# Performance work log

Hardware: AMD Instinct MI355X
Metric: run time of the kernel (lower is better)

## Reference

```python
import jax, jax.numpy as jnp
import numpy as np

B, S, D, DO, L, E = 8, 2048, 256, 256, 8, 32768


def setup_inputs() -> dict:
    key = jax.random.key(0)
    k1, k2, k3, k4, k5, k6 = jax.random.split(key, 6)
    node_repr = jax.random.normal(k1, (B, S, D), dtype=jnp.float32)
    edge_src = jax.random.randint(k2, (B, E), 0, S, dtype=jnp.int32)
    edge_tgt = jax.random.randint(k3, (B, E), 0, S, dtype=jnp.int32)
    edge_label = jax.random.randint(k4, (B, E), 0, L, dtype=jnp.int32)
    # per-label Linear params (torch default: kaiming-ish uniform; values here are random stand-ins)
    bound = 1.0 / np.sqrt(D)
    W = jax.random.uniform(k5, (L, D, DO), dtype=jnp.float32, minval=-bound, maxval=bound)
    b = jax.random.uniform(k6, (L, DO), dtype=jnp.float32, minval=-bound, maxval=bound)
    return {"node_repr": node_repr, "edge_src": edge_src, "edge_tgt": edge_tgt,
            "edge_label": edge_label, "W": W, "b": b}


def reference(node_repr, edge_src, edge_tgt, edge_label, W, b):
    # Transform every node by every label's linear once: y[b,l,s,:] = x[b,s,:] @ W[l] + b[l]
    y = jnp.einsum('bsd,ldo->blso', node_repr, W) + b[None, :, None, :]  # [B,L,S,DO]
    bidx = jnp.arange(node_repr.shape[0])[:, None]                       # [B,1]
    msgs = y[bidx, edge_label, edge_src]                                 # [B,E,DO] gather
    out = jnp.zeros(node_repr.shape[:2] + (W.shape[-1],), dtype=node_repr.dtype)
    out = out.at[bidx, edge_tgt].add(msgs)                               # scatter-add into targets
    return jax.nn.relu(out)
```

## Files before the change

### kernel.cpp

```cpp
#include <hip/hip_runtime.h>
#include <stdint.h>

constexpr int NB = 8;
constexpr int NS = 2048;
constexpr int ND = 256;
constexpr int NDO = 256;
constexpr int NL = 8;
constexpr int NE = 32768;
constexpr int K2 = NL * ND;
constexpr int CAP = 32;

typedef __attribute__((ext_vector_type(8))) short bf16x8;
typedef __attribute__((ext_vector_type(4))) float f32x4;
typedef unsigned int u32;

__device__ __forceinline__ float bf2f(uint32_t u) {
    return __uint_as_float(u << 16);
}
__device__ __forceinline__ uint16_t f2bf(float f) {
    uint32_t x = __float_as_uint(f);
    uint32_t r = (x + 0x7fffu + ((x >> 16) & 1u)) >> 16;
    return (uint16_t)r;
}

__device__ __forceinline__ void gl_lds16(const void* gptr, void* lptr) {
    __builtin_amdgcn_global_load_lds(
        (const __attribute__((address_space(1))) u32*)gptr,
        (__attribute__((address_space(3))) u32*)lptr, 16, 0, 0);
}

__global__ __launch_bounds__(256) void part_kernel(
    const float* __restrict__ W, ushort* __restrict__ wt2,
    const int* __restrict__ esrc, const int* __restrict__ etgt,
    const int* __restrict__ elab,
    int* __restrict__ cursor, ushort* __restrict__ bucket) {
    int bid = blockIdx.x;
    int tid = threadIdx.x;
    if (bid < 1024) {
        int i = bid * 256 + tid;
        int b = i >> 15;
        int c = (b << 14) + etgt[i] * NL + elab[i];
        int p = atomicAdd(&cursor[c], 1);
        if (p < CAP) bucket[(size_t)c * CAP + p] = (ushort)esrc[i];
    } else {
        __shared__ float tile[64][65];
        int tb = bid - 1024;
        int kt = tb & 31, ot = tb >> 5;
        int k0 = kt * 64, o0 = ot * 64;
        int rr = tid >> 6;
        int cc = tid & 63;
        for (int r16 = 0; r16 < 16; r16++) {
            int row = r16 * 4 + rr;
            tile[row][cc] = W[(size_t)(k0 + row) * NDO + o0 + cc];
        }
        __syncthreads();
        for (int r16 = 0; r16 < 16; r16++) {
            int orow = r16 * 4 + rr;
            wt2[(size_t)(o0 + orow) * K2 + k0 + cc] = f2bf(tile[cc][orow]);
        }
    }
}

__global__ __launch_bounds__(256) void agg_kernel(
    const float* __restrict__ x,
    const int* __restrict__ cursor, const ushort* __restrict__ bucket,
    ushort* __restrict__ Z) {
    int bid = blockIdx.x;
    int b = bid & 7;
    int lane = threadIdx.x & 63;
    int t = (bid >> 3) * 4 + (threadIdx.x >> 6);
    int g = b * NS + t;

    int cv = (lane < 8) ? cursor[(g << 3) + lane] : 0;

    const ushort* bp = bucket + (size_t)g * (NL * CAP);
    int my[4];
#pragma unroll
    for (int c = 0; c < 4; c++) my[c] = bp[c * 64 + lane];

    const float4* x4 = (const float4*)x + (size_t)b * NS * 64;
    ushort* zrow = Z + (size_t)g * K2;

#pragma unroll
    for (int l = 0; l < 8; l++) {
        int n = __shfl(cv, l);
        if (n > CAP) n = CAP;
        float4 a; a.x = a.y = a.z = a.w = 0.f;
        for (int q = 0; q < n; q++) {
            int src = __shfl(my[l >> 1], (l & 1) * CAP + q);
            float4 xv = x4[(size_t)src * 64 + lane];
            a.x += xv.x; a.y += xv.y; a.z += xv.z; a.w += xv.w;
        }
        ushort4 ob;
        ob.x = f2bf(a.x); ob.y = f2bf(a.y); ob.z = f2bf(a.z); ob.w = f2bf(a.w);
        ((ushort4*)(zrow + l * ND))[lane] = ob;
    }
}

__global__ __launch_bounds__(256, 4) void gemm2_kernel(
    const ushort* __restrict__ Z, const ushort* __restrict__ wt2,
    const int* __restrict__ cursor, const float* __restrict__ bias,
    float* __restrict__ out) {
    int bid = blockIdx.x;
    int wgid = (bid & 7) * 128 + (bid >> 3);
    int mt = wgid >> 2;
    int n0 = (wgid & 3) * 64;
    int m0 = mt * 64;

    __shared__ ushort As[64 * 64];
    __shared__ ushort Bs[64 * 64];
    __shared__ int cnt_s[64 * 8];
    __shared__ float bias_s[8 * 64];

    int tid = threadIdx.x;
    int lane = tid & 63;
    int wave = __builtin_amdgcn_readfirstlane(tid >> 6);
    int wm = wave & 1, wn = wave >> 1;
    int ln = lane & 15, quad = lane >> 4;

    {
        int e = tid * 2;
        *(int2*)&cnt_s[e] = *(const int2*)&cursor[(size_t)m0 * 8 + e];
        int l = e >> 6, col = e & 63;
        *(float2*)&bias_s[e] = *(const float2*)&bias[l * NDO + n0 + col];
    }

    f32x4 acc[2][2] = {};

    const ushort* Ag = Z + (size_t)m0 * K2;
    const ushort* Bg = wt2 + (size_t)n0 * K2;

    for (int k0 = 0; k0 < K2; k0 += 64) {
#pragma unroll
        for (int p = 0; p < 2; p++) {
            int cid = p * 256 + tid;
            int r = cid >> 3, ch = (cid & 7) ^ (r & 7);
            gl_lds16(Ag + (size_t)r * K2 + k0 + ch * 8, &As[(p * 256 + wave * 64) * 8]);
        }
#pragma unroll
        for (int p = 0; p < 2; p++) {
            int cid = p * 256 + tid;
            int r = cid >> 3, ch = (cid & 7) ^ (r & 7);
            gl_lds16(Bg + (size_t)r * K2 + k0 + ch * 8, &Bs[(p * 256 + wave * 64) * 8]);
        }
        __syncthreads();

#pragma unroll
        for (int ks = 0; ks < 2; ks++) {
            bf16x8 af[2], bfr[2];
#pragma unroll
            for (int i = 0; i < 2; i++) {
                int row = wm * 32 + i * 16 + ln;
                int ci = (ks * 4 + quad) ^ (row & 7);
                af[i] = *(const bf16x8*)&As[row * 64 + ci * 8];
            }
#pragma unroll
            for (int j = 0; j < 2; j++) {
                int row = wn * 32 + j * 16 + ln;
                int ci = (ks * 4 + quad) ^ (row & 7);
                bfr[j] = *(const bf16x8*)&Bs[row * 64 + ci * 8];
            }
#pragma unroll
            for (int i = 0; i < 2; i++)
#pragma unroll
                for (int j = 0; j < 2; j++)
                    acc[i][j] = __builtin_amdgcn_mfma_f32_16x16x32_bf16(
                        af[i], bfr[j], acc[i][j], 0, 0, 0);
        }
        __syncthreads();
    }

#pragma unroll
    for (int i = 0; i < 2; i++) {
#pragma unroll
        for (int r = 0; r < 4; r++) {
            int row_l = wm * 32 + i * 16 + quad * 4 + r;
            float cw[8];
#pragma unroll
            for (int l = 0; l < 8; l++) cw[l] = (float)cnt_s[row_l * 8 + l];
#pragma unroll
            for (int j = 0; j < 2; j++) {
                int col_l = wn * 32 + j * 16 + ln;
                float bs = 0.f;
#pragma unroll
                for (int l = 0; l < 8; l++) bs += cw[l] * bias_s[l * 64 + col_l];
                float v = acc[i][j][r] + bs;
                out[(size_t)(m0 + row_l) * NDO + n0 + col_l] = fmaxf(v, 0.f);
            }
        }
    }
}

extern "C" void kernel_launch(void* const* d_in, const int* in_sizes, int n_in,
                              void* d_out, int out_size, void* d_ws, size_t ws_size,
                              hipStream_t stream) {
    const float* x    = (const float*)d_in[0];
    const int*   esrc = (const int*)d_in[1];
    const int*   etgt = (const int*)d_in[2];
    const int*   elab = (const int*)d_in[3];
    const float* W    = (const float*)d_in[4];
    const float* bias = (const float*)d_in[5];
    float* out = (float*)d_out;

    char* ws = (char*)d_ws;
    ushort* wt2    = (ushort*)(ws);
    int*    cursor = (int*)(ws + 1048576);
    ushort* bucket = (ushort*)(ws + 1572864);
    ushort* Z      = (ushort*)(ws + 10485760);

    hipMemsetAsync(cursor, 0, NB * NS * NL * sizeof(int), stream);
    part_kernel<<<1152, 256, 0, stream>>>(W, wt2, esrc, etgt, elab, cursor, bucket);
    agg_kernel<<<4096, 256, 0, stream>>>(x, cursor, bucket, Z);
    gemm2_kernel<<<1024, 256, 0, stream>>>(Z, wt2, cursor, bias, out);
}
```

Before: 136.5 us.

## Double-buffer GEMM LDS tiles, pair label loops in aggregation, interleave partition batches

The GEMM kernel now double-buffers the A/B LDS tiles, prefetching the next K-tile with global_load_lds while MFMAs run on the current one, so each K step needs one barrier instead of two. The aggregation kernel handles two labels per iteration with independent accumulators, putting more gather loads in flight per wave. The partition kernel maps consecutive blocks to different batches, which spreads atomics across the cursor array. These changes double the GEMM's LDS use, which may cut occupancy. The double-buffering also leans on the single trailing barrier to order the async LDS writes against reads of the other buffer.

```diff
diff --git a/kernel.cpp b/kernel.cpp
--- a/kernel.cpp
+++ b/kernel.cpp
@@ -37,8 +37,8 @@
     int bid = blockIdx.x;
     int tid = threadIdx.x;
     if (bid < 1024) {
-        int i = bid * 256 + tid;
-        int b = i >> 15;
+        int b = bid & 7;
+        int i = b * NE + (bid >> 3) * 256 + tid;
         int c = (b << 14) + etgt[i] * NL + elab[i];
         int p = atomicAdd(&cursor[c], 1);
         if (p < CAP) bucket[(size_t)c * CAP + p] = (ushort)esrc[i];
@@ -82,18 +82,30 @@
     ushort* zrow = Z + (size_t)g * K2;
 
 #pragma unroll
-    for (int l = 0; l < 8; l++) {
-        int n = __shfl(cv, l);
-        if (n > CAP) n = CAP;
-        float4 a; a.x = a.y = a.z = a.w = 0.f;
-        for (int q = 0; q < n; q++) {
-            int src = __shfl(my[l >> 1], (l & 1) * CAP + q);
-            float4 xv = x4[(size_t)src * 64 + lane];
-            a.x += xv.x; a.y += xv.y; a.z += xv.z; a.w += xv.w;
+    for (int lp = 0; lp < 4; lp++) {
+        int n0 = __shfl(cv, 2 * lp);     if (n0 > CAP) n0 = CAP;
+        int n1 = __shfl(cv, 2 * lp + 1); if (n1 > CAP) n1 = CAP;
+        int ch = my[lp];
+        float4 a0 = {0.f, 0.f, 0.f, 0.f};
+        float4 a1 = {0.f, 0.f, 0.f, 0.f};
+        int nm = (n0 > n1) ? n0 : n1;
+        for (int q = 0; q < nm; q++) {
+            if (q < n0) {
+                int src = __shfl(ch, q);
+                float4 v = x4[(size_t)src * 64 + lane];
+                a0.x += v.x; a0.y += v.y; a0.z += v.z; a0.w += v.w;
+            }
+            if (q < n1) {
+                int src = __shfl(ch, 32 + q);
+                float4 v = x4[(size_t)src * 64 + lane];
+                a1.x += v.x; a1.y += v.y; a1.z += v.z; a1.w += v.w;
+            }
         }
         ushort4 ob;
-        ob.x = f2bf(a.x); ob.y = f2bf(a.y); ob.z = f2bf(a.z); ob.w = f2bf(a.w);
-        ((ushort4*)(zrow + l * ND))[lane] = ob;
+        ob.x = f2bf(a0.x); ob.y = f2bf(a0.y); ob.z = f2bf(a0.z); ob.w = f2bf(a0.w);
+        ((ushort4*)(zrow + (2 * lp) * ND))[lane] = ob;
+        ob.x = f2bf(a1.x); ob.y = f2bf(a1.y); ob.z = f2bf(a1.z); ob.w = f2bf(a1.w);
+        ((ushort4*)(zrow + (2 * lp + 1) * ND))[lane] = ob;
     }
 }
 
@@ -107,8 +119,8 @@
     int n0 = (wgid & 3) * 64;
     int m0 = mt * 64;
 
-    __shared__ ushort As[64 * 64];
-    __shared__ ushort Bs[64 * 64];
+    __shared__ ushort As[2][64 * 64];
+    __shared__ ushort Bs[2][64 * 64];
     __shared__ int cnt_s[64 * 8];
     __shared__ float bias_s[8 * 64];
 
@@ -125,25 +137,30 @@
         *(float2*)&bias_s[e] = *(const float2*)&bias[l * NDO + n0 + col];
     }
 
-    f32x4 acc[2][2] = {};
-
     const ushort* Ag = Z + (size_t)m0 * K2;
     const ushort* Bg = wt2 + (size_t)n0 * K2;
 
-    for (int k0 = 0; k0 < K2; k0 += 64) {
-#pragma unroll
-        for (int p = 0; p < 2; p++) {
-            int cid = p * 256 + tid;
-            int r = cid >> 3, ch = (cid & 7) ^ (r & 7);
-            gl_lds16(Ag + (size_t)r * K2 + k0 + ch * 8, &As[(p * 256 + wave * 64) * 8]);
-        }
-#pragma unroll
-        for (int p = 0; p < 2; p++) {
-            int cid = p * 256 + tid;
-            int r = cid >> 3, ch = (cid & 7) ^ (r & 7);
-            gl_lds16(Bg + (size_t)r * K2 + k0 + ch * 8, &Bs[(p * 256 + wave * 64) * 8]);
-        }
-        __syncthreads();
+#define STAGE(buf, k0g)                                                          \
+    do {                                                                         \
+        _Pragma("unroll")                                                        \
+        for (int p = 0; p < 2; p++) {                                            \
+            int cid = p * 256 + tid;                                             \
+            int r = cid >> 3, ch = (cid & 7) ^ (r & 7);                          \
+            gl_lds16(Ag + (size_t)r * K2 + (k0g) + ch * 8,                       \
+                     &As[buf][(p * 256 + wave * 64) * 8]);                       \
+            gl_lds16(Bg + (size_t)r * K2 + (k0g) + ch * 8,                       \
+                     &Bs[buf][(p * 256 + wave * 64) * 8]);                       \
+        }                                                                        \
+    } while (0)
+
+    f32x4 acc[2][2] = {};
+
+    STAGE(0, 0);
+    __syncthreads();
+
+    for (int kt = 0; kt < K2 / 64; kt++) {
+        int cur = kt & 1;
+        if (kt + 1 < K2 / 64) STAGE(cur ^ 1, (kt + 1) * 64);
 
 #pragma unroll
         for (int ks = 0; ks < 2; ks++) {
@@ -152,13 +169,13 @@
             for (int i = 0; i < 2; i++) {
                 int row = wm * 32 + i * 16 + ln;
                 int ci = (ks * 4 + quad) ^ (row & 7);
-                af[i] = *(const bf16x8*)&As[row * 64 + ci * 8];
+                af[i] = *(const bf16x8*)&As[cur][row * 64 + ci * 8];
             }
 #pragma unroll
             for (int j = 0; j < 2; j++) {
                 int row = wn * 32 + j * 16 + ln;
                 int ci = (ks * 4 + quad) ^ (row & 7);
-                bfr[j] = *(const bf16x8*)&Bs[row * 64 + ci * 8];
+                bfr[j] = *(const bf16x8*)&Bs[cur][row * 64 + ci * 8];
             }
 #pragma unroll
             for (int i = 0; i < 2; i++)
@@ -169,6 +186,7 @@
         }
         __syncthreads();
     }
+#undef STAGE
 
 #pragma unroll
     for (int i = 0; i < 2; i++) {
```

After: 136.6 us. No clear change (+0.1%).
